# Optimization experiments

Hardware: AMD Instinct MI355X
Metric: run time of the kernel (lower is better)

## Reference

```python
import jax, jax.numpy as jnp
import numpy as np

B, S, E, D = 8, 2048, 1024, 64


def setup_inputs() -> dict:
    key = jax.random.key(0)
    ks = jax.random.split(key, 8)
    x = jax.random.normal(ks[0], (B, S, E), dtype=jnp.float32)
    mask = jax.random.randint(ks[1], (B, S), 0, 2, dtype=jnp.int32)
    # torch.nn.Linear(E, D): weight [D, E], bias [D]; y = x @ W.T + b
    scale = 0.02
    Wq = jax.random.normal(ks[2], (D, E), dtype=jnp.float32) * scale
    bq = jax.random.normal(ks[3], (D,), dtype=jnp.float32) * scale
    Wk = jax.random.normal(ks[4], (D, E), dtype=jnp.float32) * scale
    bk = jax.random.normal(ks[5], (D,), dtype=jnp.float32) * scale
    Wv = jax.random.normal(ks[6], (D, E), dtype=jnp.float32) * scale
    bv = jax.random.normal(ks[7], (D,), dtype=jnp.float32) * scale
    return {"x": x, "mask": mask, "Wq": Wq, "bq": bq, "Wk": Wk, "bk": bk, "Wv": Wv, "bv": bv}


def reference(x, mask, Wq, bq, Wk, bk, Wv, bv):
    # Linear projections: [B,S,E] @ [E,D] -> [B,S,D]
    q = jnp.einsum('bse,de->bsd', x, Wq) + bq
    k = jnp.einsum('bse,de->bsd', x, Wk) + bk
    v = jnp.einsum('bse,de->bsd', x, Wv) + bv
    # scores: [B,S,S]
    scores = jnp.einsum('bid,bjd->bij', q, k) / np.sqrt(D).astype(np.float32)
    # Faithful mask replication: temp_mask[b,i,j] = mask[b,j] if j >= i else 0;
    # positions where temp_mask == 0 are filled with -1e22 (training=True).
    seq = scores.shape[1]
    upper = jnp.triu(jnp.ones((seq, seq), dtype=bool))        # j >= i
    valid = upper[None, :, :] & (mask[:, None, :] != 0)        # [B,S,S]
    scores = jnp.where(valid, scores, jnp.float32(-1e22))
    attn = jax.nn.softmax(scores, axis=-1)
    # out: [B,S,D]
    return jnp.einsum('bij,bjd->bid', attn, v)
```

## Files before the change

### kernel.cpp

```cpp
#include <hip/hip_runtime.h>
#include <hip/hip_bf16.h>

#define NB 8
#define NS 2048
#define NE 1024
#define ND 64

typedef __attribute__((ext_vector_type(8))) short bf16x8;
typedef __attribute__((ext_vector_type(4))) float f32x4;
typedef unsigned short u16;
typedef unsigned long long u64;

#define MFMA(a, b, c) __builtin_amdgcn_mfma_f32_16x16x32_bf16(a, b, c, 0, 0, 0)

__device__ __forceinline__ u16 f2bf(float f) {
  unsigned int u = __float_as_uint(f);
  u += 0x7fffu + ((u >> 16) & 1u);
  return (u16)(u >> 16);
}
__device__ __forceinline__ unsigned cvt2(float a, float b) {
  __hip_bfloat162 h = __float22bfloat162_rn(float2{a, b});
  return *(unsigned*)&h;
}

__device__ __forceinline__ void alds16(const void* g, void* l) {
  __builtin_amdgcn_global_load_lds(
      (const __attribute__((address_space(1))) unsigned int*)g,
      (__attribute__((address_space(3))) unsigned int*)l, 16, 0, 0);
}

__global__ void k0_prep(const float* __restrict__ Wq, const float* __restrict__ bq,
                        const float* __restrict__ Wk, const float* __restrict__ bk,
                        const float* __restrict__ Wv, const float* __restrict__ bv,
                        u16* __restrict__ Wcat2, float* __restrict__ bcat,
                        float* __restrict__ vmean) {
  int d = blockIdx.x * 256 + threadIdx.x;
  int c = d / 1536;
  int rem = d - c * 1536;
  int n = rem >> 3;
  int qp = rem & 7;
  int q = qp ^ (n & 7);
  const float* src = (n < 64) ? (Wq + n * NE) : (n < 128) ? (Wk + (n - 64) * NE)
                                                          : (Wv + (n - 128) * NE);
  const float* sp = src + c * 64 + q * 8;
  float4 a = *(const float4*)sp;
  float4 b = *(const float4*)(sp + 4);
  bf16x8 o;
  o[0] = (short)f2bf(a.x); o[1] = (short)f2bf(a.y);
  o[2] = (short)f2bf(a.z); o[3] = (short)f2bf(a.w);
  o[4] = (short)f2bf(b.x); o[5] = (short)f2bf(b.y);
  o[6] = (short)f2bf(b.z); o[7] = (short)f2bf(b.w);
  *(bf16x8*)&Wcat2[(size_t)d * 8] = o;
  if (blockIdx.x == 0) {
    int t = threadIdx.x;
    if (t < 192) bcat[t] = (t < 64) ? bq[t] : (t < 128) ? bk[t - 64] : bv[t - 128];
    vmean[t] = 0.f;
    vmean[t + 256] = 0.f;
  }
}

__global__ __launch_bounds__(256) void k1_qkv(
    const float* __restrict__ x, const u16* __restrict__ Wcat2,
    const float* __restrict__ bcat, u16* __restrict__ qb,
    u16* __restrict__ kbf2, u16* __restrict__ vtb2, float* __restrict__ vmean) {
  __shared__ float axs[2][32 * 64];
  __shared__ u16 bsb[2][192 * 64];
  const int t = threadIdx.x;
  const int m0 = blockIdx.x * 32;
  const int batch = m0 >> 11;
  const int sl = m0 & (NS - 1);
  const int w = t >> 6;
  const int l = t & 63;
  const int ln = l & 15;
  const int qd = l >> 4;
  const int n0 = w * 48;

  f32x4 zf = {0.f, 0.f, 0.f, 0.f};
  f32x4 acc[2][3] = {{zf, zf, zf}, {zf, zf, zf}};

  auto stageA = [&](int c, int buf) {
    #pragma unroll
    for (int i = 0; i < 2; ++i) {
      int rr = w * 8 + i * 4 + (l >> 4);
      int gch = (l & 15) ^ (rr & 7);
      const float* gp = x + (size_t)(m0 + rr) * NE + c * 64 + gch * 4;
      alds16(gp, &axs[buf][(w * 8 + i * 4) * 64]);
    }
  };
  auto stageB = [&](int c, int buf) {
    const u16* cb = Wcat2 + (size_t)c * 12288;
    #pragma unroll
    for (int i = 0; i < 6; ++i) {
      const u16* gp = cb + (w * 6 + i) * 512 + l * 8;
      alds16(gp, &bsb[buf][(w * 6 + i) * 512]);
    }
  };

  stageA(0, 0);
  stageB(0, 0);

  for (int c = 0; c < 16; ++c) {
    __syncthreads();
    if (c < 15) { stageA(c + 1, (c + 1) & 1); stageB(c + 1, (c + 1) & 1); }
    const int buf = c & 1;
    const int s = ln & 7;
    bf16x8 afr[2][2];
    #pragma unroll
    for (int mi = 0; mi < 2; ++mi) {
      int row = mi * 16 + ln;
      #pragma unroll
      for (int kc = 0; kc < 2; ++kc) {
        int g0 = kc * 8 + qd * 2;
        float4 fa = *(const float4*)&axs[buf][row * 64 + ((g0 ^ s) * 4)];
        float4 fb = *(const float4*)&axs[buf][row * 64 + (((g0 + 1) ^ s) * 4)];
        union { bf16x8 v; unsigned u[4]; } A;
        A.u[0] = cvt2(fa.x, fa.y); A.u[1] = cvt2(fa.z, fa.w);
        A.u[2] = cvt2(fb.x, fb.y); A.u[3] = cvt2(fb.z, fb.w);
        afr[mi][kc] = A.v;
      }
    }
    #pragma unroll
    for (int kc = 0; kc < 2; ++kc)
      #pragma unroll
      for (int nj = 0; nj < 3; ++nj) {
        int n = n0 + nj * 16 + ln;
        bf16x8 bb = *(const bf16x8*)&bsb[buf][n * 64 + (((kc * 4 + qd) ^ s) * 8)];
        acc[0][nj] = MFMA(afr[0][kc], bb, acc[0][nj]);
        acc[1][nj] = MFMA(afr[1][kc], bb, acc[1][nj]);
      }
  }

  #pragma unroll
  for (int nj = 0; nj < 3; ++nj) {
    int n = n0 + nj * 16 + ln;
    float bias = bcat[n];
    #pragma unroll
    for (int mi = 0; mi < 2; ++mi) {
      int jbase = sl + mi * 16 + qd * 4;
      if (n < 64) {
        #pragma unroll
        for (int r = 0; r < 4; ++r)
          qb[((size_t)batch * NS + jbase + r) * ND + n] = f2bf(acc[mi][nj][r] + bias);
      } else if (n < 128) {
        int d = n - 64;
        #pragma unroll
        for (int r = 0; r < 4; ++r) {
          int j = jbase + r;
          int pos = (((d >> 3) ^ (j & 7)) << 3) + (d & 7);
          kbf2[((size_t)batch * NS + j) * ND + pos] = f2bf(acc[mi][nj][r] + bias);
        }
      } else {
        int d = n - 128;
        int off = (jbase & ~63) + (((((jbase >> 5) & 1) ^ ((d >> 2) & 1))) << 5) +
                  (((((jbase >> 3) & 3) ^ (d & 3))) << 3) + (jbase & 7);
        ushort4 sv;
        sv.x = f2bf(acc[mi][nj][0] + bias); sv.y = f2bf(acc[mi][nj][1] + bias);
        sv.z = f2bf(acc[mi][nj][2] + bias); sv.w = f2bf(acc[mi][nj][3] + bias);
        *(ushort4*)&vtb2[((size_t)batch * ND + d) * NS + off] = sv;
      }
    }
    if (n >= 128) {
      float psum = acc[0][nj][0] + acc[0][nj][1] + acc[0][nj][2] + acc[0][nj][3] +
                   acc[1][nj][0] + acc[1][nj][1] + acc[1][nj][2] + acc[1][nj][3] +
                   8.f * bias;
      psum += __shfl_xor(psum, 16);
      psum += __shfl_xor(psum, 32);
      if (l < 16) atomicAdd(&vmean[batch * ND + (n - 128)], psum * (1.f / 2048.f));
    }
  }
}

__global__ __launch_bounds__(512, 4) void k3_attn(
    const u16* __restrict__ qb, const u16* __restrict__ kbf2,
    const u16* __restrict__ vtb2, const int* __restrict__ mask,
    const float* __restrict__ vmean, float* __restrict__ out) {
  __shared__ u16 ks[2][128 * 64];
  __shared__ u16 vs[2][64 * 128];
  __shared__ union {
    u16 ps[8][16 * 40];
    struct { float mb[2][16][68]; float mlb[2][16][16]; } m;
  } ub;

  const int g = blockIdx.x;
  const int tl = g >> 3;
  const int b = g & 7;
  const int i0 = tl * 32;
  const int j0f = i0 & ~127;
  const int np = (NS - j0f) >> 7;
  const int t = threadIdx.x;
  const int w = t >> 6;
  const int l = t & 63;
  const int ln = l & 15;
  const int qd = l >> 4;
  const int rg = w & 1;
  const int jg = w >> 1;

  const u16* qp = qb + ((size_t)b * NS + i0 + rg * 16 + ln) * ND + qd * 8;
  bf16x8 aq0 = *(const bf16x8*)qp;
  bf16x8 aq1 = *(const bf16x8*)(qp + 32);

  const u16* kB = kbf2 + (size_t)b * NS * ND;
  const u16* vB = vtb2 + (size_t)b * ND * NS;

  auto stage = [&](int it, int buf) {
    int j0 = j0f + it * 128;
    #pragma unroll
    for (int i = 0; i < 2; ++i) {
      int jl = w * 16 + i * 8;
      alds16(kB + (size_t)(j0 + jl) * ND + l * 8, &ks[buf][jl * 64]);
      int du = w * 2 + i;
      alds16(vB + (size_t)(du * 4 + (l >> 4)) * NS + j0 + (l & 15) * 8,
             &vs[buf][du * 512]);
    }
  };

  f32x4 zf = {0.f, 0.f, 0.f, 0.f};
  f32x4 od[4] = {zf, zf, zf, zf};
  float ls[4] = {0.f, 0.f, 0.f, 0.f};

  stage(0, 0);
  int mval = mask[b * NS + j0f + jg * 32 + (l & 31)];

  for (int it = 0; it < np; ++it) {
    u64 mv = __ballot(mval != 0);
    __syncthreads();
    if (it + 1 < np) {
      stage(it + 1, (it + 1) & 1);
      mval = mask[b * NS + j0f + (it + 1) * 128 + jg * 32 + (l & 31)];
    }
    const int buf = it & 1;
    const int jb = j0f + it * 128 + jg * 32;

    f32x4 sc[2] = {zf, zf};
    #pragma unroll
    for (int f = 0; f < 2; ++f) {
      const u16* kr = &ks[buf][(jg * 32 + f * 16 + ln) * 64];
      bf16x8 b0 = *(const bf16x8*)&kr[((qd ^ (ln & 7)) * 8)];
      bf16x8 b1 = *(const bf16x8*)&kr[(((4 + qd) ^ (ln & 7)) * 8)];
      sc[f] = MFMA(aq0, b0, sc[f]);
      sc[f] = MFMA(aq1, b1, sc[f]);
    }
    #pragma unroll
    for (int r = 0; r < 4; ++r) {
      const int i = i0 + rg * 16 + qd * 4 + r;
      #pragma unroll
      for (int f = 0; f < 2; ++f) {
        int jl = f * 16 + ln;
        bool ok = ((jb + jl) >= i) && (((mv >> jl) & 1ull) != 0);
        float p = ok ? __expf(sc[f][r] * 0.125f) : 0.f;
        ls[r] += p;
        ub.ps[w][(qd * 4 + r) * 40 + jl] = f2bf(p);
      }
    }
    bf16x8 pa = *(const bf16x8*)&ub.ps[w][ln * 40 + qd * 8];
    #pragma unroll
    for (int gx = 0; gx < 4; ++gx) {
      int unit = (jg >> 1) * 8 + (((jg & 1) ^ ((ln >> 2) & 1)) << 2) + (qd ^ (ln & 3));
      bf16x8 bv = *(const bf16x8*)&vs[buf][(gx * 16 + ln) * 128 + unit * 8];
      od[gx] = MFMA(pa, bv, od[gx]);
    }
  }

  __syncthreads();
  #pragma unroll 1
  for (int s = 3; s >= 1; --s) {
    if (jg == s) {
      #pragma unroll
      for (int r = 0; r < 4; ++r) {
        int row = qd * 4 + r;
        #pragma unroll
        for (int gx = 0; gx < 4; ++gx) ub.m.mb[rg][row][gx * 16 + ln] = od[gx][r];
        ub.m.mlb[rg][row][ln] = ls[r];
      }
    }
    __syncthreads();
    if (jg == s - 1) {
      #pragma unroll
      for (int r = 0; r < 4; ++r) {
        int row = qd * 4 + r;
        #pragma unroll
        for (int gx = 0; gx < 4; ++gx) od[gx][r] += ub.m.mb[rg][row][gx * 16 + ln];
        ls[r] += ub.m.mlb[rg][row][ln];
      }
    }
    __syncthreads();
  }

  if (jg == 0) {
    #pragma unroll
    for (int r = 0; r < 4; ++r) {
      #pragma unroll
      for (int o = 1; o < 16; o <<= 1) ls[r] += __shfl_xor(ls[r], o);
      int row = i0 + rg * 16 + qd * 4 + r;
      float* orow = out + ((size_t)b * NS + row) * ND;
      if (ls[r] > 0.f) {
        float inv = 1.f / ls[r];
        #pragma unroll
        for (int gx = 0; gx < 4; ++gx) orow[gx * 16 + ln] = od[gx][r] * inv;
      } else {
        #pragma unroll
        for (int gx = 0; gx < 4; ++gx) orow[gx * 16 + ln] = vmean[b * ND + gx * 16 + ln];
      }
    }
  }
}

extern "C" void kernel_launch(void* const* d_in, const int* in_sizes, int n_in,
                              void* d_out, int out_size, void* d_ws, size_t ws_size,
                              hipStream_t stream) {
  (void)in_sizes; (void)n_in; (void)out_size; (void)ws_size;
  const float* x = (const float*)d_in[0];
  const int* mask = (const int*)d_in[1];
  const float* Wq = (const float*)d_in[2];
  const float* bq = (const float*)d_in[3];
  const float* Wk = (const float*)d_in[4];
  const float* bk = (const float*)d_in[5];
  const float* Wv = (const float*)d_in[6];
  const float* bv = (const float*)d_in[7];
  float* out = (float*)d_out;

  char* ws = (char*)d_ws;
  u16* Wcat2 = (u16*)ws;
  float* bcat = (float*)(ws + 393216);
  float* vmean = (float*)(ws + 394240);
  u16* qb = (u16*)(ws + (1u << 20));
  u16* kbf2 = (u16*)(ws + (3u << 20));
  u16* vtb2 = (u16*)(ws + (5u << 20));

  hipLaunchKernelGGL(k0_prep, dim3(96), dim3(256), 0, stream,
                     Wq, bq, Wk, bk, Wv, bv, Wcat2, bcat, vmean);
  hipLaunchKernelGGL(k1_qkv, dim3(512), dim3(256), 0, stream,
                     x, Wcat2, bcat, qb, kbf2, vtb2, vmean);
  hipLaunchKernelGGL(k3_attn, dim3(512), dim3(512), 0, stream,
                     qb, kbf2, vtb2, mask, vmean, out);
}
```

Measured before the change: 146.3 us.

## Compute transposed scores and build P operand in registers via permlane swaps

Swaps the MFMA operands so the score tile comes out transposed (keys along rows, query per lane). The P fragment for the PV MFMA is then built in registers with v_permlane32/16_swap instead of a round trip through shared memory. The causal check is only evaluated on the first (diagonal) tile; later tiles apply the key mask as an additive bias before the exp. Row sums become per-lane scalars reduced with shuffles, which shrinks the LDS reduction buffer. This removes the per-iteration LDS write/read and its bank traffic, at the cost of relying on gfx950 permlane instructions and a correct lane mapping.

```diff
diff --git a/kernel.cpp b/kernel.cpp
--- a/kernel.cpp
+++ b/kernel.cpp
@@ -21,6 +21,13 @@
 __device__ __forceinline__ unsigned cvt2(float a, float b) {
   __hip_bfloat162 h = __float22bfloat162_rn(float2{a, b});
   return *(unsigned*)&h;
+}
+
+__device__ __forceinline__ void pl32swap(unsigned& a, unsigned& b) {
+  asm("v_permlane32_swap_b32 %0, %1" : "+v"(a), "+v"(b));
+}
+__device__ __forceinline__ void pl16swap(unsigned& a, unsigned& b) {
+  asm("v_permlane16_swap_b32 %0, %1" : "+v"(a), "+v"(b));
 }
 
 __device__ __forceinline__ void alds16(const void* g, void* l) {
@@ -176,10 +183,7 @@
     const float* __restrict__ vmean, float* __restrict__ out) {
   __shared__ u16 ks[2][128 * 64];
   __shared__ u16 vs[2][64 * 128];
-  __shared__ union {
-    u16 ps[8][16 * 40];
-    struct { float mb[2][16][68]; float mlb[2][16][16]; } m;
-  } ub;
+  __shared__ struct { float mb[2][16][68]; float mlb[2][16]; } ub;
 
   const int g = blockIdx.x;
   const int tl = g >> 3;
@@ -216,7 +220,7 @@
 
   f32x4 zf = {0.f, 0.f, 0.f, 0.f};
   f32x4 od[4] = {zf, zf, zf, zf};
-  float ls[4] = {0.f, 0.f, 0.f, 0.f};
+  float ls0 = 0.f, ls1 = 0.f;
 
   stage(0, 0);
   int mval = mask[b * NS + j0f + jg * 32 + (l & 31)];
@@ -231,28 +235,51 @@
     const int buf = it & 1;
     const int jb = j0f + it * 128 + jg * 32;
 
-    f32x4 sc[2] = {zf, zf};
+    f32x4 sT[2] = {zf, zf};
     #pragma unroll
     for (int f = 0; f < 2; ++f) {
       const u16* kr = &ks[buf][(jg * 32 + f * 16 + ln) * 64];
       bf16x8 b0 = *(const bf16x8*)&kr[((qd ^ (ln & 7)) * 8)];
       bf16x8 b1 = *(const bf16x8*)&kr[(((4 + qd) ^ (ln & 7)) * 8)];
-      sc[f] = MFMA(aq0, b0, sc[f]);
-      sc[f] = MFMA(aq1, b1, sc[f]);
-    }
-    #pragma unroll
-    for (int r = 0; r < 4; ++r) {
-      const int i = i0 + rg * 16 + qd * 4 + r;
-      #pragma unroll
-      for (int f = 0; f < 2; ++f) {
-        int jl = f * 16 + ln;
-        bool ok = ((jb + jl) >= i) && (((mv >> jl) & 1ull) != 0);
-        float p = ok ? __expf(sc[f][r] * 0.125f) : 0.f;
-        ls[r] += p;
-        ub.ps[w][(qd * 4 + r) * 40 + jl] = f2bf(p);
-      }
-    }
-    bf16x8 pa = *(const bf16x8*)&ub.ps[w][ln * 40 + qd * 8];
+      sT[f] = MFMA(b0, aq0, sT[f]);
+      sT[f] = MFMA(b1, aq1, sT[f]);
+    }
+
+    unsigned mq = (unsigned)(mv >> (qd * 4));
+    float p[2][4];
+    if (it == 0) {
+      const int di = jb + qd * 4 - (i0 + rg * 16 + ln);
+      #pragma unroll
+      for (int f = 0; f < 2; ++f)
+        #pragma unroll
+        for (int r = 0; r < 4; ++r) {
+          bool ok = (((mq >> (16 * f + r)) & 1u) != 0) && (di + 16 * f + r >= 0);
+          p[f][r] = ok ? __expf(sT[f][r] * 0.125f) : 0.f;
+        }
+    } else {
+      #pragma unroll
+      for (int f = 0; f < 2; ++f)
+        #pragma unroll
+        for (int r = 0; r < 4; ++r) {
+          float bias = ((mq >> (16 * f + r)) & 1u) ? 0.f : -1e30f;
+          p[f][r] = __expf(__builtin_fmaf(sT[f][r], 0.125f, bias));
+        }
+    }
+    ls0 += p[0][0] + p[0][1] + p[0][2] + p[0][3];
+    ls1 += p[1][0] + p[1][1] + p[1][2] + p[1][3];
+
+    unsigned x00 = cvt2(p[0][0], p[0][1]);
+    unsigned x01 = cvt2(p[0][2], p[0][3]);
+    unsigned x10 = cvt2(p[1][0], p[1][1]);
+    unsigned x11 = cvt2(p[1][2], p[1][3]);
+    pl32swap(x00, x10);
+    pl32swap(x01, x11);
+    pl16swap(x00, x10);
+    pl16swap(x01, x11);
+    union { bf16x8 v; unsigned u[4]; } PA;
+    PA.u[0] = x00; PA.u[1] = x01; PA.u[2] = x10; PA.u[3] = x11;
+    bf16x8 pa = PA.v;
+
     #pragma unroll
     for (int gx = 0; gx < 4; ++gx) {
       int unit = (jg >> 1) * 8 + (((jg & 1) ^ ((ln >> 2) & 1)) << 2) + (qd ^ (ln & 3));
@@ -261,7 +288,10 @@
     }
   }
 
-  __syncthreads();
+  float ls = ls0 + ls1;
+  ls += __shfl_xor(ls, 16);
+  ls += __shfl_xor(ls, 32);
+
   #pragma unroll 1
   for (int s = 3; s >= 1; --s) {
     if (jg == s) {
@@ -269,9 +299,9 @@
       for (int r = 0; r < 4; ++r) {
         int row = qd * 4 + r;
         #pragma unroll
-        for (int gx = 0; gx < 4; ++gx) ub.m.mb[rg][row][gx * 16 + ln] = od[gx][r];
-        ub.m.mlb[rg][row][ln] = ls[r];
-      }
+        for (int gx = 0; gx < 4; ++gx) ub.mb[rg][row][gx * 16 + ln] = od[gx][r];
+      }
+      if (qd == 0) ub.mlb[rg][ln] = ls;
     }
     __syncthreads();
     if (jg == s - 1) {
@@ -279,9 +309,9 @@
       for (int r = 0; r < 4; ++r) {
         int row = qd * 4 + r;
         #pragma unroll
-        for (int gx = 0; gx < 4; ++gx) od[gx][r] += ub.m.mb[rg][row][gx * 16 + ln];
-        ls[r] += ub.m.mlb[rg][row][ln];
-      }
+        for (int gx = 0; gx < 4; ++gx) od[gx][r] += ub.mb[rg][row][gx * 16 + ln];
+      }
+      ls += ub.mlb[rg][ln];
     }
     __syncthreads();
   }
@@ -289,12 +319,11 @@
   if (jg == 0) {
     #pragma unroll
     for (int r = 0; r < 4; ++r) {
-      #pragma unroll
-      for (int o = 1; o < 16; o <<= 1) ls[r] += __shfl_xor(ls[r], o);
+      float lr = __shfl(ls, qd * 4 + r);
       int row = i0 + rg * 16 + qd * 4 + r;
       float* orow = out + ((size_t)b * NS + row) * ND;
-      if (ls[r] > 0.f) {
-        float inv = 1.f / ls[r];
+      if (lr > 0.f) {
+        float inv = 1.f / lr;
         #pragma unroll
         for (int gx = 0; gx < 4; ++gx) orow[gx * 16 + ln] = od[gx][r] * inv;
       } else {
```

After: 143.5 us. No clear change (-1.9%).
